# Kernel tuning notes

Measured on AMD Instinct MI355X. Metric: run time of the kernel, lower is better.

Reference implementation:

```python
import jax, jax.numpy as jnp
import numpy as np

B, S, D, H = 4, 2048, 1024, 16
HD = D // H


def setup_inputs() -> dict:
    key = jax.random.key(0)
    ks = jax.random.split(key, 12)
    inp = {
        "query": jax.random.normal(ks[0], (B, S, D), jnp.float32),
        "key": jax.random.normal(ks[1], (B, S, D), jnp.float32),
        "value": jax.random.normal(ks[2], (B, S, D), jnp.float32),
        "mask": jnp.tril(jnp.ones((S, S), jnp.int32)),  # causal mask
        "Wq": jax.random.normal(ks[3], (D, D), jnp.float32) / np.sqrt(D),
        "bq": jax.random.normal(ks[4], (D,), jnp.float32) * 0.02,
        "Wk": jax.random.normal(ks[5], (D, D), jnp.float32) / np.sqrt(D),
        "bk": jax.random.normal(ks[6], (D,), jnp.float32) * 0.02,
        "Wv": jax.random.normal(ks[7], (D, D), jnp.float32) / np.sqrt(D),
        "bv": jax.random.normal(ks[8], (D,), jnp.float32) * 0.02,
        "Wo": jax.random.normal(ks[9], (D, D), jnp.float32) / np.sqrt(D),
        "bo": jax.random.normal(ks[10], (D,), jnp.float32) * 0.02,
    }
    return inp


def reference(query, key, value, mask, Wq, bq, Wk, bk, Wv, bv, Wo, bo):
    # Linear projections (torch nn.Linear: y = x @ W.T + b)
    q = query @ Wq.T + bq
    k = key @ Wk.T + bk
    v = value @ Wv.T + bv
    # split heads: [B, S, D] -> [B, H, S, HD]
    q = q.reshape(B, S, H, HD).transpose(0, 2, 1, 3)
    k = k.reshape(B, S, H, HD).transpose(0, 2, 1, 3)
    v = v.reshape(B, S, H, HD).transpose(0, 2, 1, 3)
    # scaled dot-product attention with full [B,H,S,S] scores (faithful to source)
    scores = jnp.einsum("bhqd,bhkd->bhqk", q, k) / jnp.sqrt(jnp.float32(HD))
    scores = jnp.where(mask == 0, -jnp.inf, scores)
    attn = jax.nn.softmax(scores, axis=-1)
    out = jnp.einsum("bhqk,bhkd->bhqd", attn, v)
    # merge heads and output projection (dropout rate = 0.0 -> identity)
    out = out.transpose(0, 2, 1, 3).reshape(B, S, D)
    return out @ Wo.T + bo
```

## Files before the change

### kernel.cpp

```cpp
#include <hip/hip_runtime.h>

typedef __bf16 bf16x8 __attribute__((ext_vector_type(8)));
typedef __bf16 bf16x2 __attribute__((ext_vector_type(2)));
typedef float f32x4 __attribute__((ext_vector_type(4)));
typedef float f32x16 __attribute__((ext_vector_type(16)));
typedef unsigned short ushort;

__device__ __forceinline__ int4 cvt8(float4 a, float4 b) {
  bf16x8 v;
  v[0] = (__bf16)a.x; v[1] = (__bf16)a.y; v[2] = (__bf16)a.z; v[3] = (__bf16)a.w;
  v[4] = (__bf16)b.x; v[5] = (__bf16)b.y; v[6] = (__bf16)b.z; v[7] = (__bf16)b.w;
  return __builtin_bit_cast(int4, v);
}

__device__ __forceinline__ void gld16(const void* g, void* l) {
  __builtin_amdgcn_global_load_lds(
      (const __attribute__((address_space(1))) void*)g,
      (__attribute__((address_space(3))) void*)l, 16, 0, 0);
}

__device__ __forceinline__ unsigned pkbf(float a, float b) {
  bf16x2 v;
  v[0] = (__bf16)a;
  v[1] = (__bf16)b;
  return __builtin_bit_cast(unsigned, v);
}

#if __has_builtin(__builtin_amdgcn_permlane32_swap)
typedef unsigned u32x2 __attribute__((ext_vector_type(2)));
__device__ __forceinline__ void plswap(unsigned& a, unsigned& b, int hi) {
  (void)hi;
  u32x2 r = __builtin_amdgcn_permlane32_swap(a, b, false, false);
  a = r[0]; b = r[1];
}
#else
__device__ __forceinline__ void plswap(unsigned& a, unsigned& b, int hi) {
  const unsigned pa = (unsigned)__shfl_xor((int)a, 32);
  const unsigned pb = (unsigned)__shfl_xor((int)b, 32);
  const unsigned x = hi ? pb : a;
  const unsigned y = hi ? b : pa;
  a = x; b = y;
}
#endif

__device__ __forceinline__ f32x16 mfma32(bf16x8 a, bf16x8 b, f32x16 c) {
  return __builtin_amdgcn_mfma_f32_32x32x16_bf16(a, b, c, 0, 0, 0);
}

__global__ __launch_bounds__(256) void cvt4_k(const float* __restrict__ i0,
                                              const float* __restrict__ i1,
                                              const float* __restrict__ i2,
                                              const float* __restrict__ i3,
                                              ushort* __restrict__ o, int n8) {
  const int z = blockIdx.y;
  const float* in = (z == 0) ? i0 : (z == 1) ? i1 : (z == 2) ? i2 : i3;
  ushort* out = o + (size_t)z * 1024 * 1024;
  int i = blockIdx.x * 256 + threadIdx.x;
  if (i >= n8) return;
  const float4* p = (const float4*)in + (size_t)i * 2;
  *(int4*)(out + (size_t)i * 8) = cvt8(p[0], p[1]);
}

template <int AMODE, int WMODE, int OMODE>
__global__ __launch_bounds__(256) void gemm_k(const void* __restrict__ A,
                                              const void* __restrict__ W,
                                              const float* __restrict__ bias,
                                              void* __restrict__ Out,
                                              float oscale) {
  constexpr int K = 1024;
  __shared__ __align__(16) char lA[128 * 128];
  __shared__ __align__(16) char lB[128 * 128];
  const int t = threadIdx.x;
  const int l = t & 63;
  const int w = t >> 6;
  const int wr = w >> 1, wc = w & 1;
  const int m0 = blockIdx.x * 128;
  const int n0 = blockIdx.y * 128;
  const int srow = l >> 3;
  const int scol = ((l & 7) ^ srow) << 3;
  f32x4 acc[4][4];
#pragma unroll
  for (int i = 0; i < 4; ++i)
#pragma unroll
    for (int j = 0; j < 4; ++j) acc[i][j] = (f32x4){0.f, 0.f, 0.f, 0.f};

  for (int k0 = 0; k0 < K; k0 += 64) {
    if constexpr (AMODE == 1) {
#pragma unroll
      for (int i = 0; i < 4; ++i) {
        const int chunk = w * 4 + i;
        gld16((const ushort*)A + (size_t)(m0 + chunk * 8 + srow) * K + k0 + scol,
              lA + chunk * 1024);
      }
    } else {
#pragma unroll
      for (int qq = 0; qq < 4; ++qq) {
        const int L = t * 8 + qq * 2048;
        const int r = L >> 6, c = L & 63;
        const int dst = r * 128 + ((c * 2) ^ ((r & 7) << 4));
        const float* s0 = (const float*)A + (size_t)(m0 + r) * K + k0 + c;
        *(int4*)(lA + dst) = cvt8(*(const float4*)s0, *(const float4*)(s0 + 4));
      }
    }
    if constexpr (WMODE == 1) {
#pragma unroll
      for (int i = 0; i < 4; ++i) {
        const int chunk = w * 4 + i;
        gld16((const ushort*)W + (size_t)(n0 + chunk * 8 + srow) * K + k0 + scol,
              lB + chunk * 1024);
      }
    } else {
#pragma unroll
      for (int qq = 0; qq < 4; ++qq) {
        const int L = t * 8 + qq * 2048;
        const int r = L >> 6, c = L & 63;
        const int dst = r * 128 + ((c * 2) ^ ((r & 7) << 4));
        const float* s1 = (const float*)W + (size_t)(n0 + r) * K + k0 + c;
        *(int4*)(lB + dst) = cvt8(*(const float4*)s1, *(const float4*)(s1 + 4));
      }
    }
    __syncthreads();
#pragma unroll
    for (int ks = 0; ks < 2; ++ks) {
      const int kb = ks * 64 + ((l >> 4) << 4);
      bf16x8 af[4], bfv[4];
#pragma unroll
      for (int i = 0; i < 4; ++i) {
        const int row = wr * 64 + i * 16 + (l & 15);
        af[i] = *(const bf16x8*)(lA + row * 128 + (kb ^ ((row & 7) << 4)));
      }
#pragma unroll
      for (int j = 0; j < 4; ++j) {
        const int row = wc * 64 + j * 16 + (l & 15);
        bfv[j] = *(const bf16x8*)(lB + row * 128 + (kb ^ ((row & 7) << 4)));
      }
#pragma unroll
      for (int i = 0; i < 4; ++i)
#pragma unroll
        for (int j = 0; j < 4; ++j)
          acc[i][j] = __builtin_amdgcn_mfma_f32_16x16x32_bf16(af[i], bfv[j],
                                                              acc[i][j], 0, 0, 0);
    }
    __syncthreads();
  }
#pragma unroll
  for (int i = 0; i < 4; ++i)
#pragma unroll
    for (int j = 0; j < 4; ++j)
#pragma unroll
      for (int rg = 0; rg < 4; ++rg) {
        const int gm = m0 + wr * 64 + i * 16 + ((l >> 4) << 2) + rg;
        const int gn = n0 + wc * 64 + j * 16 + (l & 15);
        const float v = (acc[i][j][rg] + bias[gn]) * oscale;
        if constexpr (OMODE == 0) {
          const int b = gm >> 11, s = gm & 2047, h = gn >> 6, hd = gn & 63;
          ((ushort*)Out)[((((size_t)(b * 16 + h)) * 2048 + s) << 6) + hd] =
              __builtin_bit_cast(ushort, (__bf16)v);
        } else if constexpr (OMODE == 1) {
          const int b = gm >> 11, s = gm & 2047, h = gn >> 6, hd = gn & 63;
          ((ushort*)Out)[((((size_t)(b * 16 + h)) << 6) + hd) * 2048 + s] =
              __builtin_bit_cast(ushort, (__bf16)v);
        } else {
          ((float*)Out)[(size_t)gm * 1024 + gn] = v;
        }
      }
}

__global__ __launch_bounds__(256) void attn_k(const ushort* __restrict__ qh,
                                              const ushort* __restrict__ kh,
                                              const ushort* __restrict__ vth,
                                              ushort* __restrict__ out) {
  const int bh = blockIdx.x;
  const int qt = gridDim.y - 1 - blockIdx.y;
  const int q0 = qt * 128;
  const int t = threadIdx.x, l = t & 63, wv = t >> 6;
  const int lq = l & 31, hi = l >> 5;
  __shared__ __align__(16) char lk[2][64 * 128];
  __shared__ __align__(16) char lv[2][64 * 128];

  const int qrow = q0 + wv * 32 + lq;
  bf16x8 qf0, qf1, qf2, qf3;
  {
    const ushort* qp = qh + ((size_t)bh * 2048 + qrow) * 64 + hi * 8;
    qf0 = *(const bf16x8*)(qp);
    qf1 = *(const bf16x8*)(qp + 16);
    qf2 = *(const bf16x8*)(qp + 32);
    qf3 = *(const bf16x8*)(qp + 48);
  }
  bf16x8 ones8;
#pragma unroll
  for (int i = 0; i < 8; ++i) ones8[i] = (__bf16)1.0f;

  const int r0 = t >> 3;
  const int c0 = (t & 7) * 8;
  const ushort* kbase = kh + (size_t)bh * 2048 * 64 + (size_t)r0 * 64 + c0;
  const ushort* vbase = vth + (size_t)bh * 64 * 2048 + (size_t)r0 * 2048 + c0;
  const int dst0 = r0 * 128 + ((c0 * 2) ^ ((r0 & 7) << 4));

  int4 ka, kb2, va, vb2;
#define LOAD_TILE(kv0)                                            \
  do {                                                            \
    ka  = *(const int4*)(kbase + (size_t)(kv0) * 64);             \
    kb2 = *(const int4*)(kbase + (size_t)(kv0) * 64 + 32 * 64);   \
    va  = *(const int4*)(vbase + (kv0));                          \
    vb2 = *(const int4*)(vbase + (kv0) + 32 * 2048);              \
  } while (0)
#define WRITE_TILE(buf)                                           \
  do {                                                            \
    *(int4*)(lk[buf] + dst0) = ka;                                \
    *(int4*)(lk[buf] + dst0 + 32 * 128) = kb2;                    \
    *(int4*)(lv[buf] + dst0) = va;                                \
    *(int4*)(lv[buf] + dst0 + 32 * 128) = vb2;                    \
  } while (0)

  LOAD_TILE(0);
  WRITE_TILE(0);

  float m_r = -1e30f;
  f32x16 acco[2];
  f32x16 acc_l;
#pragma unroll
  for (int dt = 0; dt < 2; ++dt)
#pragma unroll
    for (int r = 0; r < 16; ++r) acco[dt][r] = 0.f;
#pragma unroll
  for (int r = 0; r < 16; ++r) acc_l[r] = 0.f;

  const int nt = 2 * qt + 2;
  int cur = 0;
#pragma unroll 1
  for (int ti = 0; ti < nt; ++ti) {
    __syncthreads();
    if (ti + 1 < nt) LOAD_TILE((ti + 1) << 6);

#pragma unroll
    for (int s = 0; s < 2; ++s) {
      const int kvs = (ti << 6) + s * 32;
      if (kvs > q0 + wv * 32 + 31) continue;

      f32x16 p;
#pragma unroll
      for (int r = 0; r < 16; ++r) p[r] = 0.f;
#pragma unroll
      for (int kd = 0; kd < 4; ++kd) {
        const int row = s * 32 + lq;
        const bf16x8 kf = *(const bf16x8*)(
            lk[cur] + row * 128 + ((kd * 32 + hi * 16) ^ ((row & 7) << 4)));
        const bf16x8 qf = (kd == 0) ? qf0 : (kd == 1) ? qf1 : (kd == 2) ? qf2 : qf3;
        p = mfma32(kf, qf, p);
      }
      if (kvs + 31 > q0 + wv * 32) {
#pragma unroll
        for (int r = 0; r < 16; ++r) {
          const int kv = kvs + (r & 3) + 8 * (r >> 2) + 4 * hi;
          if (kv > qrow) p[r] = -1e30f;
        }
      }
      const float a0 = fmaxf(fmaxf(p[0], p[1]), p[2]);
      const float a1 = fmaxf(fmaxf(p[3], p[4]), p[5]);
      const float a2 = fmaxf(fmaxf(p[6], p[7]), p[8]);
      const float a3 = fmaxf(fmaxf(p[9], p[10]), p[11]);
      const float a4 = fmaxf(fmaxf(p[12], p[13]), p[14]);
      const float b0 = fmaxf(fmaxf(a0, a1), a2);
      const float b1 = fmaxf(fmaxf(a3, a4), p[15]);
      float tm = fmaxf(b0, b1);
      tm = fmaxf(tm, __shfl_xor(tm, 32));
      if (!__all(tm <= m_r + 8.f)) {
        const float mn = fmaxf(m_r, tm);
        const float e = __builtin_amdgcn_exp2f(m_r - mn);
        m_r = mn;
#pragma unroll
        for (int dt = 0; dt < 2; ++dt)
#pragma unroll
          for (int r = 0; r < 16; ++r) acco[dt][r] *= e;
#pragma unroll
        for (int r = 0; r < 16; ++r) acc_l[r] *= e;
      }
#pragma unroll
      for (int r = 0; r < 16; ++r) p[r] = __builtin_amdgcn_exp2f(p[r] - m_r);
      unsigned W0a = pkbf(p[0], p[1]),   W0b = pkbf(p[2], p[3]);
      unsigned W1a = pkbf(p[4], p[5]),   W1b = pkbf(p[6], p[7]);
      unsigned W2a = pkbf(p[8], p[9]),   W2b = pkbf(p[10], p[11]);
      unsigned W3a = pkbf(p[12], p[13]), W3b = pkbf(p[14], p[15]);
#pragma unroll
      for (int ks = 0; ks < 2; ++ks) {
        unsigned a0u = ks ? W2a : W0a;
        unsigned a1u = ks ? W2b : W0b;
        unsigned b0u = ks ? W3a : W1a;
        unsigned b1u = ks ? W3b : W1b;
        plswap(a0u, b0u, hi);
        plswap(a1u, b1u, hi);
        const uint4 pw = {a0u, a1u, b0u, b1u};
        const bf16x8 pf = __builtin_bit_cast(bf16x8, pw);
        acc_l = mfma32(ones8, pf, acc_l);
#pragma unroll
        for (int dt = 0; dt < 2; ++dt) {
          const int row = dt * 32 + lq;
          const bf16x8 vf = *(const bf16x8*)(
              lv[cur] + row * 128 +
              ((s * 64 + ks * 32 + hi * 16) ^ ((row & 7) << 4)));
          acco[dt] = mfma32(vf, pf, acco[dt]);
        }
      }
    }
    if (ti + 1 < nt) WRITE_TILE(cur ^ 1);
    cur ^= 1;
  }
#undef LOAD_TILE
#undef WRITE_TILE
  const int b = bh >> 4, h = bh & 15;
  const float inv = __builtin_amdgcn_rcpf(acc_l[0]);
  ushort* orow = out + ((size_t)(b * 2048 + qrow)) * 1024 + h * 64;
#pragma unroll
  for (int dt = 0; dt < 2; ++dt)
#pragma unroll
    for (int g = 0; g < 4; ++g) {
      ushort4 st;
      st.x = __builtin_bit_cast(ushort, (__bf16)(acco[dt][4 * g + 0] * inv));
      st.y = __builtin_bit_cast(ushort, (__bf16)(acco[dt][4 * g + 1] * inv));
      st.z = __builtin_bit_cast(ushort, (__bf16)(acco[dt][4 * g + 2] * inv));
      st.w = __builtin_bit_cast(ushort, (__bf16)(acco[dt][4 * g + 3] * inv));
      *(ushort4*)(orow + dt * 32 + g * 8 + hi * 4) = st;
    }
}

extern "C" void kernel_launch(void* const* d_in, const int* in_sizes, int n_in,
                              void* d_out, int out_size, void* d_ws, size_t ws_size,
                              hipStream_t stream) {
  (void)in_sizes; (void)n_in; (void)out_size;
  const float* query = (const float*)d_in[0];
  const float* key = (const float*)d_in[1];
  const float* value = (const float*)d_in[2];
  const float* Wq = (const float*)d_in[4];
  const float* bq = (const float*)d_in[5];
  const float* Wk = (const float*)d_in[6];
  const float* bk = (const float*)d_in[7];
  const float* Wv = (const float*)d_in[8];
  const float* bv = (const float*)d_in[9];
  const float* Wo = (const float*)d_in[10];
  const float* bo = (const float*)d_in[11];

  char* ws = (char*)d_ws;
  const size_t SZA = (size_t)8192 * 1024 * 2;
  const size_t SZW = (size_t)1024 * 1024 * 2;
  ushort* qh = (ushort*)(ws + 0 * SZA);
  ushort* kh = (ushort*)(ws + 1 * SZA);
  ushort* vt = (ushort*)(ws + 2 * SZA);
  ushort* ao = (ushort*)(ws + 3 * SZA);
  dim3 bb(256), gg(64, 8), ga(64, 16);
  const float QS = 0.125f * 1.44269504088896f;

  if (ws_size >= 4 * SZA + 4 * SZW) {
    ushort* wq = (ushort*)(ws + 4 * SZA);
    ushort* wk = (ushort*)(ws + 4 * SZA + 1 * SZW);
    ushort* wv = (ushort*)(ws + 4 * SZA + 2 * SZW);
    ushort* wo = (ushort*)(ws + 4 * SZA + 3 * SZW);
    const int n8w = 1024 * 1024 / 8;
    hipLaunchKernelGGL(cvt4_k, dim3(n8w / 256, 4), bb, 0, stream, Wq, Wk, Wv, Wo, wq, n8w);
    hipLaunchKernelGGL((gemm_k<0, 1, 0>), gg, bb, 0, stream, (const void*)query, (const void*)wq, bq, (void*)qh, QS);
    hipLaunchKernelGGL((gemm_k<0, 1, 0>), gg, bb, 0, stream, (const void*)key, (const void*)wk, bk, (void*)kh, 1.0f);
    hipLaunchKernelGGL((gemm_k<0, 1, 1>), gg, bb, 0, stream, (const void*)value, (const void*)wv, bv, (void*)vt, 1.0f);
    hipLaunchKernelGGL(attn_k, ga, bb, 0, stream, qh, kh, vt, ao);
    hipLaunchKernelGGL((gemm_k<1, 1, 2>), gg, bb, 0, stream, (const void*)ao, (const void*)wo, bo, d_out, 1.0f);
  } else {
    hipLaunchKernelGGL((gemm_k<0, 0, 0>), gg, bb, 0, stream, (const void*)query, (const void*)Wq, bq, (void*)qh, QS);
    hipLaunchKernelGGL((gemm_k<0, 0, 0>), gg, bb, 0, stream, (const void*)key, (const void*)Wk, bk, (void*)kh, 1.0f);
    hipLaunchKernelGGL((gemm_k<0, 0, 1>), gg, bb, 0, stream, (const void*)value, (const void*)Wv, bv, (void*)vt, 1.0f);
    hipLaunchKernelGGL(attn_k, ga, bb, 0, stream, qh, kh, vt, ao);
    hipLaunchKernelGGL((gemm_k<1, 0, 2>), gg, bb, 0, stream, (const void*)ao, (const void*)Wo, bo, d_out, 1.0f);
  }
}
```

Baseline: 198.6 us.

## Merge QKV projections into one launch and rebalance causal attention blocks

The three input projections become a single launch with a z-dimension selecting Q/K/V, which cuts launch overhead and fills more of the GPU at once. Attention moves to 128-thread blocks with 64-row query tiles. Each block handles two tiles, one from the top and one from the bottom of the sequence, so causal work is balanced across blocks. The row-sum is now computed with shuffles and adds instead of an extra MFMA against a ones vector. The fallback path is restructured into a float-weight GEMM. Smaller attention blocks may lower per-block reuse of the K/V tiles held in LDS.

```diff
diff --git a/kernel.cpp b/kernel.cpp
--- a/kernel.cpp
+++ b/kernel.cpp
@@ -61,12 +61,305 @@
   *(int4*)(out + (size_t)i * 8) = cvt8(p[0], p[1]);
 }
 
-template <int AMODE, int WMODE, int OMODE>
-__global__ __launch_bounds__(256) void gemm_k(const void* __restrict__ A,
-                                              const void* __restrict__ W,
-                                              const float* __restrict__ bias,
-                                              void* __restrict__ Out,
-                                              float oscale) {
+template <int AMODE>
+__device__ __forceinline__ void gemm_body(const void* __restrict__ A,
+                                          const ushort* __restrict__ W,
+                                          const float* __restrict__ bias,
+                                          void* __restrict__ Out, float oscale,
+                                          int omode, char* lA, char* lB) {
+  constexpr int K = 1024;
+  const int t = threadIdx.x;
+  const int l = t & 63;
+  const int w = t >> 6;
+  const int wr = w >> 1, wc = w & 1;
+  const int m0 = blockIdx.x * 128;
+  const int n0 = blockIdx.y * 128;
+  const int srow = l >> 3;
+  const int scol = ((l & 7) ^ srow) << 3;
+  f32x4 acc[4][4];
+#pragma unroll
+  for (int i = 0; i < 4; ++i)
+#pragma unroll
+    for (int j = 0; j < 4; ++j) acc[i][j] = (f32x4){0.f, 0.f, 0.f, 0.f};
+
+  for (int k0 = 0; k0 < K; k0 += 64) {
+    if constexpr (AMODE == 1) {
+#pragma unroll
+      for (int i = 0; i < 4; ++i) {
+        const int chunk = w * 4 + i;
+        gld16((const ushort*)A + (size_t)(m0 + chunk * 8 + srow) * K + k0 + scol,
+              lA + chunk * 1024);
+      }
+    } else {
+#pragma unroll
+      for (int qq = 0; qq < 4; ++qq) {
+        const int L = t * 8 + qq * 2048;
+        const int r = L >> 6, c = L & 63;
+        const int dst = r * 128 + ((c * 2) ^ ((r & 7) << 4));
+        const float* s0 = (const float*)A + (size_t)(m0 + r) * K + k0 + c;
+        *(int4*)(lA + dst) = cvt8(*(const float4*)s0, *(const float4*)(s0 + 4));
+      }
+    }
+#pragma unroll
+    for (int i = 0; i < 4; ++i) {
+      const int chunk = w * 4 + i;
+      gld16(W + (size_t)(n0 + chunk * 8 + srow) * K + k0 + scol, lB + chunk * 1024);
+    }
+    __syncthreads();
+#pragma unroll
+    for (int ks = 0; ks < 2; ++ks) {
+      const int kb = ks * 64 + ((l >> 4) << 4);
+      bf16x8 af[4], bfv[4];
+#pragma unroll
+      for (int i = 0; i < 4; ++i) {
+        const int row = wr * 64 + i * 16 + (l & 15);
+        af[i] = *(const bf16x8*)(lA + row * 128 + (kb ^ ((row & 7) << 4)));
+      }
+#pragma unroll
+      for (int j = 0; j < 4; ++j) {
+        const int row = wc * 64 + j * 16 + (l & 15);
+        bfv[j] = *(const bf16x8*)(lB + row * 128 + (kb ^ ((row & 7) << 4)));
+      }
+#pragma unroll
+      for (int i = 0; i < 4; ++i)
+#pragma unroll
+        for (int j = 0; j < 4; ++j)
+          acc[i][j] = __builtin_amdgcn_mfma_f32_16x16x32_bf16(af[i], bfv[j],
+                                                              acc[i][j], 0, 0, 0);
+    }
+    __syncthreads();
+  }
+#pragma unroll
+  for (int i = 0; i < 4; ++i)
+#pragma unroll
+    for (int j = 0; j < 4; ++j)
+#pragma unroll
+      for (int rg = 0; rg < 4; ++rg) {
+        const int gm = m0 + wr * 64 + i * 16 + ((l >> 4) << 2) + rg;
+        const int gn = n0 + wc * 64 + j * 16 + (l & 15);
+        const float v = (acc[i][j][rg] + bias[gn]) * oscale;
+        if (omode == 0) {
+          const int b = gm >> 11, s = gm & 2047, h = gn >> 6, hd = gn & 63;
+          ((ushort*)Out)[((((size_t)(b * 16 + h)) * 2048 + s) << 6) + hd] =
+              __builtin_bit_cast(ushort, (__bf16)v);
+        } else if (omode == 1) {
+          const int b = gm >> 11, s = gm & 2047, h = gn >> 6, hd = gn & 63;
+          ((ushort*)Out)[((((size_t)(b * 16 + h)) << 6) + hd) * 2048 + s] =
+              __builtin_bit_cast(ushort, (__bf16)v);
+        } else {
+          ((float*)Out)[(size_t)gm * 1024 + gn] = v;
+        }
+      }
+}
+
+__global__ __launch_bounds__(256) void gemmQKV_k(
+    const float* __restrict__ Aq, const float* __restrict__ Ak,
+    const float* __restrict__ Av, const ushort* __restrict__ Wb,
+    const float* __restrict__ bq, const float* __restrict__ bk,
+    const float* __restrict__ bv, ushort* __restrict__ qh,
+    ushort* __restrict__ kh, ushort* __restrict__ vt, float qs) {
+  __shared__ __align__(16) char lA[128 * 128];
+  __shared__ __align__(16) char lB[128 * 128];
+  const int z = blockIdx.z;
+  const float* A = (z == 0) ? Aq : (z == 1) ? Ak : Av;
+  const float* bias = (z == 0) ? bq : (z == 1) ? bk : bv;
+  void* Out = (z == 0) ? (void*)qh : (z == 1) ? (void*)kh : (void*)vt;
+  gemm_body<0>(A, Wb + (size_t)z * 1024 * 1024, bias, Out,
+               (z == 0) ? qs : 1.0f, (z == 2) ? 1 : 0, lA, lB);
+}
+
+__global__ __launch_bounds__(256) void gemmO_k(const ushort* __restrict__ A,
+                                               const ushort* __restrict__ W,
+                                               const float* __restrict__ bias,
+                                               float* __restrict__ Out) {
+  __shared__ __align__(16) char lA[128 * 128];
+  __shared__ __align__(16) char lB[128 * 128];
+  gemm_body<1>(A, W, bias, Out, 1.0f, 2, lA, lB);
+}
+
+__global__ __launch_bounds__(128) void attn_k(const ushort* __restrict__ qh,
+                                              const ushort* __restrict__ kh,
+                                              const ushort* __restrict__ vth,
+                                              ushort* __restrict__ out) {
+  const int bh = blockIdx.x;
+  const int t = threadIdx.x, l = t & 63, wv = t >> 6;
+  const int lq = l & 31, hi = l >> 5;
+  __shared__ __align__(16) char lk[2][64 * 128];
+  __shared__ __align__(16) char lv[2][64 * 128];
+
+  const int r0 = t >> 1;
+  const int cq = (t & 1) * 32;
+  const ushort* kbase = kh + (size_t)bh * 2048 * 64 + (size_t)r0 * 64 + cq;
+  const ushort* vbase = vth + (size_t)bh * 64 * 2048 + (size_t)r0 * 2048 + cq;
+  const int swz = (r0 & 7) << 4;
+  const int d0 = r0 * 128 + ((cq * 2 + 0) ^ swz);
+  const int d1 = r0 * 128 + ((cq * 2 + 16) ^ swz);
+  const int d2 = r0 * 128 + ((cq * 2 + 32) ^ swz);
+  const int d3 = r0 * 128 + ((cq * 2 + 48) ^ swz);
+  const int b = bh >> 4, h = bh & 15;
+
+  int4 ka0, ka1, ka2, ka3, va0, va1, va2, va3;
+#define LOAD_TILE(kv0)                                      \
+  do {                                                      \
+    const ushort* kp = kbase + (size_t)(kv0) * 64;          \
+    const ushort* vp = vbase + (kv0);                       \
+    ka0 = *(const int4*)(kp);                               \
+    ka1 = *(const int4*)(kp + 8);                           \
+    ka2 = *(const int4*)(kp + 16);                          \
+    ka3 = *(const int4*)(kp + 24);                          \
+    va0 = *(const int4*)(vp);                               \
+    va1 = *(const int4*)(vp + 8);                           \
+    va2 = *(const int4*)(vp + 16);                          \
+    va3 = *(const int4*)(vp + 24);                          \
+  } while (0)
+#define WRITE_TILE(buf)                                     \
+  do {                                                      \
+    *(int4*)(lk[buf] + d0) = ka0;                           \
+    *(int4*)(lk[buf] + d1) = ka1;                           \
+    *(int4*)(lk[buf] + d2) = ka2;                           \
+    *(int4*)(lk[buf] + d3) = ka3;                           \
+    *(int4*)(lv[buf] + d0) = va0;                           \
+    *(int4*)(lv[buf] + d1) = va1;                           \
+    *(int4*)(lv[buf] + d2) = va2;                           \
+    *(int4*)(lv[buf] + d3) = va3;                           \
+  } while (0)
+
+#pragma unroll 1
+  for (int pass = 0; pass < 2; ++pass) {
+    const int qt = pass ? blockIdx.y : (31 - blockIdx.y);
+    const int q0 = qt * 64;
+    const int qwave = q0 + wv * 32;
+    const int qrow = qwave + lq;
+
+    bf16x8 qf0, qf1, qf2, qf3;
+    {
+      const ushort* qp = qh + ((size_t)bh * 2048 + qrow) * 64 + hi * 8;
+      qf0 = *(const bf16x8*)(qp);
+      qf1 = *(const bf16x8*)(qp + 16);
+      qf2 = *(const bf16x8*)(qp + 32);
+      qf3 = *(const bf16x8*)(qp + 48);
+    }
+    LOAD_TILE(0);
+    __syncthreads();
+    WRITE_TILE(0);
+
+    float m_r = -1e30f, l_r = 0.f;
+    f32x16 acco[2];
+#pragma unroll
+    for (int dt = 0; dt < 2; ++dt)
+#pragma unroll
+      for (int r = 0; r < 16; ++r) acco[dt][r] = 0.f;
+
+    const int nt = qt + 1;
+    int cur = 0;
+#pragma unroll 1
+    for (int ti = 0; ti < nt; ++ti) {
+      __syncthreads();
+      if (ti + 1 < nt) LOAD_TILE((ti + 1) << 6);
+
+#pragma unroll
+      for (int s = 0; s < 2; ++s) {
+        const int kvs = (ti << 6) + s * 32;
+        if (kvs > qwave + 31) continue;
+
+        f32x16 p;
+#pragma unroll
+        for (int r = 0; r < 16; ++r) p[r] = 0.f;
+#pragma unroll
+        for (int kd = 0; kd < 4; ++kd) {
+          const int row = s * 32 + lq;
+          const bf16x8 kf = *(const bf16x8*)(
+              lk[cur] + row * 128 + ((kd * 32 + hi * 16) ^ ((row & 7) << 4)));
+          const bf16x8 qf = (kd == 0) ? qf0 : (kd == 1) ? qf1 : (kd == 2) ? qf2 : qf3;
+          p = mfma32(kf, qf, p);
+        }
+        if (kvs + 31 > qwave) {
+#pragma unroll
+          for (int r = 0; r < 16; ++r) {
+            const int kv = kvs + (r & 3) + 8 * (r >> 2) + 4 * hi;
+            if (kv > qrow) p[r] = -1e30f;
+          }
+        }
+        const float a0 = fmaxf(fmaxf(p[0], p[1]), p[2]);
+        const float a1 = fmaxf(fmaxf(p[3], p[4]), p[5]);
+        const float a2 = fmaxf(fmaxf(p[6], p[7]), p[8]);
+        const float a3 = fmaxf(fmaxf(p[9], p[10]), p[11]);
+        const float a4 = fmaxf(fmaxf(p[12], p[13]), p[14]);
+        const float b0 = fmaxf(fmaxf(a0, a1), a2);
+        const float b1 = fmaxf(fmaxf(a3, a4), p[15]);
+        float tm = fmaxf(b0, b1);
+        tm = fmaxf(tm, __shfl_xor(tm, 32));
+        if (!__all(tm <= m_r + 8.f)) {
+          const float mn = fmaxf(m_r, tm);
+          const float e = __builtin_amdgcn_exp2f(m_r - mn);
+          m_r = mn;
+          l_r *= e;
+#pragma unroll
+          for (int dt = 0; dt < 2; ++dt)
+#pragma unroll
+            for (int r = 0; r < 16; ++r) acco[dt][r] *= e;
+        }
+#pragma unroll
+        for (int r = 0; r < 16; ++r) p[r] = __builtin_amdgcn_exp2f(p[r] - m_r);
+        float sr[8];
+#pragma unroll
+        for (int r = 0; r < 8; ++r) sr[r] = p[r] + p[r + 8];
+#pragma unroll
+        for (int r = 0; r < 4; ++r) sr[r] = sr[r] + sr[r + 4];
+        float rs = (sr[0] + sr[1]) + (sr[2] + sr[3]);
+        rs += __shfl_xor(rs, 32);
+        l_r += rs;
+        unsigned W0a = pkbf(p[0], p[1]),   W0b = pkbf(p[2], p[3]);
+        unsigned W1a = pkbf(p[4], p[5]),   W1b = pkbf(p[6], p[7]);
+        unsigned W2a = pkbf(p[8], p[9]),   W2b = pkbf(p[10], p[11]);
+        unsigned W3a = pkbf(p[12], p[13]), W3b = pkbf(p[14], p[15]);
+#pragma unroll
+        for (int ks = 0; ks < 2; ++ks) {
+          unsigned a0u = ks ? W2a : W0a;
+          unsigned a1u = ks ? W2b : W0b;
+          unsigned b0u = ks ? W3a : W1a;
+          unsigned b1u = ks ? W3b : W1b;
+          plswap(a0u, b0u, hi);
+          plswap(a1u, b1u, hi);
+          const uint4 pw = {a0u, a1u, b0u, b1u};
+          const bf16x8 pf = __builtin_bit_cast(bf16x8, pw);
+#pragma unroll
+          for (int dt = 0; dt < 2; ++dt) {
+            const int row = dt * 32 + lq;
+            const bf16x8 vf = *(const bf16x8*)(
+                lv[cur] + row * 128 +
+                ((s * 64 + ks * 32 + hi * 16) ^ ((row & 7) << 4)));
+            acco[dt] = mfma32(vf, pf, acco[dt]);
+          }
+        }
+      }
+      if (ti + 1 < nt) WRITE_TILE(cur ^ 1);
+      cur ^= 1;
+    }
+    const float inv = __builtin_amdgcn_rcpf(l_r);
+    ushort* orow = out + ((size_t)(b * 2048 + qrow)) * 1024 + h * 64;
+#pragma unroll
+    for (int dt = 0; dt < 2; ++dt)
+#pragma unroll
+      for (int g = 0; g < 4; ++g) {
+        ushort4 st;
+        st.x = __builtin_bit_cast(ushort, (__bf16)(acco[dt][4 * g + 0] * inv));
+        st.y = __builtin_bit_cast(ushort, (__bf16)(acco[dt][4 * g + 1] * inv));
+        st.z = __builtin_bit_cast(ushort, (__bf16)(acco[dt][4 * g + 2] * inv));
+        st.w = __builtin_bit_cast(ushort, (__bf16)(acco[dt][4 * g + 3] * inv));
+        *(ushort4*)(orow + dt * 32 + g * 8 + hi * 4) = st;
+      }
+  }
+#undef LOAD_TILE
+#undef WRITE_TILE
+}
+
+template <int OMODE>
+__global__ __launch_bounds__(256) void gemmF_k(const void* __restrict__ A,
+                                               const float* __restrict__ W,
+                                               const float* __restrict__ bias,
+                                               void* __restrict__ Out,
+                                               float oscale, int amode) {
   constexpr int K = 1024;
   __shared__ __align__(16) char lA[128 * 128];
   __shared__ __align__(16) char lB[128 * 128];
@@ -76,48 +369,26 @@
   const int wr = w >> 1, wc = w & 1;
   const int m0 = blockIdx.x * 128;
   const int n0 = blockIdx.y * 128;
-  const int srow = l >> 3;
-  const int scol = ((l & 7) ^ srow) << 3;
   f32x4 acc[4][4];
 #pragma unroll
   for (int i = 0; i < 4; ++i)
 #pragma unroll
     for (int j = 0; j < 4; ++j) acc[i][j] = (f32x4){0.f, 0.f, 0.f, 0.f};
-
   for (int k0 = 0; k0 < K; k0 += 64) {
-    if constexpr (AMODE == 1) {
-#pragma unroll
-      for (int i = 0; i < 4; ++i) {
-        const int chunk = w * 4 + i;
-        gld16((const ushort*)A + (size_t)(m0 + chunk * 8 + srow) * K + k0 + scol,
-              lA + chunk * 1024);
-      }
-    } else {
-#pragma unroll
-      for (int qq = 0; qq < 4; ++qq) {
-        const int L = t * 8 + qq * 2048;
-        const int r = L >> 6, c = L & 63;
-        const int dst = r * 128 + ((c * 2) ^ ((r & 7) << 4));
+#pragma unroll
+    for (int qq = 0; qq < 4; ++qq) {
+      const int L = t * 8 + qq * 2048;
+      const int r = L >> 6, c = L & 63;
+      const int dst = r * 128 + ((c * 2) ^ ((r & 7) << 4));
+      if (amode == 0) {
         const float* s0 = (const float*)A + (size_t)(m0 + r) * K + k0 + c;
         *(int4*)(lA + dst) = cvt8(*(const float4*)s0, *(const float4*)(s0 + 4));
-      }
-    }
-    if constexpr (WMODE == 1) {
-#pragma unroll
-      for (int i = 0; i < 4; ++i) {
-        const int chunk = w * 4 + i;
-        gld16((const ushort*)W + (size_t)(n0 + chunk * 8 + srow) * K + k0 + scol,
-              lB + chunk * 1024);
-      }
-    } else {
-#pragma unroll
-      for (int qq = 0; qq < 4; ++qq) {
-        const int L = t * 8 + qq * 2048;
-        const int r = L >> 6, c = L & 63;
-        const int dst = r * 128 + ((c * 2) ^ ((r & 7) << 4));
-        const float* s1 = (const float*)W + (size_t)(n0 + r) * K + k0 + c;
-        *(int4*)(lB + dst) = cvt8(*(const float4*)s1, *(const float4*)(s1 + 4));
-      }
+      } else {
+        *(int4*)(lA + dst) =
+            *(const int4*)((const ushort*)A + (size_t)(m0 + r) * K + k0 + c);
+      }
+      const float* s1 = W + (size_t)(n0 + r) * K + k0 + c;
+      *(int4*)(lB + dst) = cvt8(*(const float4*)s1, *(const float4*)(s1 + 4));
     }
     __syncthreads();
 #pragma unroll
@@ -164,164 +435,6 @@
           ((float*)Out)[(size_t)gm * 1024 + gn] = v;
         }
       }
-}
-
-__global__ __launch_bounds__(256) void attn_k(const ushort* __restrict__ qh,
-                                              const ushort* __restrict__ kh,
-                                              const ushort* __restrict__ vth,
-                                              ushort* __restrict__ out) {
-  const int bh = blockIdx.x;
-  const int qt = gridDim.y - 1 - blockIdx.y;
-  const int q0 = qt * 128;
-  const int t = threadIdx.x, l = t & 63, wv = t >> 6;
-  const int lq = l & 31, hi = l >> 5;
-  __shared__ __align__(16) char lk[2][64 * 128];
-  __shared__ __align__(16) char lv[2][64 * 128];
-
-  const int qrow = q0 + wv * 32 + lq;
-  bf16x8 qf0, qf1, qf2, qf3;
-  {
-    const ushort* qp = qh + ((size_t)bh * 2048 + qrow) * 64 + hi * 8;
-    qf0 = *(const bf16x8*)(qp);
-    qf1 = *(const bf16x8*)(qp + 16);
-    qf2 = *(const bf16x8*)(qp + 32);
-    qf3 = *(const bf16x8*)(qp + 48);
-  }
-  bf16x8 ones8;
-#pragma unroll
-  for (int i = 0; i < 8; ++i) ones8[i] = (__bf16)1.0f;
-
-  const int r0 = t >> 3;
-  const int c0 = (t & 7) * 8;
-  const ushort* kbase = kh + (size_t)bh * 2048 * 64 + (size_t)r0 * 64 + c0;
-  const ushort* vbase = vth + (size_t)bh * 64 * 2048 + (size_t)r0 * 2048 + c0;
-  const int dst0 = r0 * 128 + ((c0 * 2) ^ ((r0 & 7) << 4));
-
-  int4 ka, kb2, va, vb2;
-#define LOAD_TILE(kv0)                                            \
-  do {                                                            \
-    ka  = *(const int4*)(kbase + (size_t)(kv0) * 64);             \
-    kb2 = *(const int4*)(kbase + (size_t)(kv0) * 64 + 32 * 64);   \
-    va  = *(const int4*)(vbase + (kv0));                          \
-    vb2 = *(const int4*)(vbase + (kv0) + 32 * 2048);              \
-  } while (0)
-#define WRITE_TILE(buf)                                           \
-  do {                                                            \
-    *(int4*)(lk[buf] + dst0) = ka;                                \
-    *(int4*)(lk[buf] + dst0 + 32 * 128) = kb2;                    \
-    *(int4*)(lv[buf] + dst0) = va;                                \
-    *(int4*)(lv[buf] + dst0 + 32 * 128) = vb2;                    \
-  } while (0)
-
-  LOAD_TILE(0);
-  WRITE_TILE(0);
-
-  float m_r = -1e30f;
-  f32x16 acco[2];
-  f32x16 acc_l;
-#pragma unroll
-  for (int dt = 0; dt < 2; ++dt)
-#pragma unroll
-    for (int r = 0; r < 16; ++r) acco[dt][r] = 0.f;
-#pragma unroll
-  for (int r = 0; r < 16; ++r) acc_l[r] = 0.f;
-
-  const int nt = 2 * qt + 2;
-  int cur = 0;
-#pragma unroll 1
-  for (int ti = 0; ti < nt; ++ti) {
-    __syncthreads();
-    if (ti + 1 < nt) LOAD_TILE((ti + 1) << 6);
-
-#pragma unroll
-    for (int s = 0; s < 2; ++s) {
-      const int kvs = (ti << 6) + s * 32;
-      if (kvs > q0 + wv * 32 + 31) continue;
-
-      f32x16 p;
-#pragma unroll
-      for (int r = 0; r < 16; ++r) p[r] = 0.f;
-#pragma unroll
-      for (int kd = 0; kd < 4; ++kd) {
-        const int row = s * 32 + lq;
-        const bf16x8 kf = *(const bf16x8*)(
-            lk[cur] + row * 128 + ((kd * 32 + hi * 16) ^ ((row & 7) << 4)));
-        const bf16x8 qf = (kd == 0) ? qf0 : (kd == 1) ? qf1 : (kd == 2) ? qf2 : qf3;
-        p = mfma32(kf, qf, p);
-      }
-      if (kvs + 31 > q0 + wv * 32) {
-#pragma unroll
-        for (int r = 0; r < 16; ++r) {
-          const int kv = kvs + (r & 3) + 8 * (r >> 2) + 4 * hi;
-          if (kv > qrow) p[r] = -1e30f;
-        }
-      }
-      const float a0 = fmaxf(fmaxf(p[0], p[1]), p[2]);
-      const float a1 = fmaxf(fmaxf(p[3], p[4]), p[5]);
-      const float a2 = fmaxf(fmaxf(p[6], p[7]), p[8]);
-      const float a3 = fmaxf(fmaxf(p[9], p[10]), p[11]);
-      const float a4 = fmaxf(fmaxf(p[12], p[13]), p[14]);
-      const float b0 = fmaxf(fmaxf(a0, a1), a2);
-      const float b1 = fmaxf(fmaxf(a3, a4), p[15]);
-      float tm = fmaxf(b0, b1);
-      tm = fmaxf(tm, __shfl_xor(tm, 32));
-      if (!__all(tm <= m_r + 8.f)) {
-        const float mn = fmaxf(m_r, tm);
-        const float e = __builtin_amdgcn_exp2f(m_r - mn);
-        m_r = mn;
-#pragma unroll
-        for (int dt = 0; dt < 2; ++dt)
-#pragma unroll
-          for (int r = 0; r < 16; ++r) acco[dt][r] *= e;
-#pragma unroll
-        for (int r = 0; r < 16; ++r) acc_l[r] *= e;
-      }
-#pragma unroll
-      for (int r = 0; r < 16; ++r) p[r] = __builtin_amdgcn_exp2f(p[r] - m_r);
-      unsigned W0a = pkbf(p[0], p[1]),   W0b = pkbf(p[2], p[3]);
-      unsigned W1a = pkbf(p[4], p[5]),   W1b = pkbf(p[6], p[7]);
-      unsigned W2a = pkbf(p[8], p[9]),   W2b = pkbf(p[10], p[11]);
-      unsigned W3a = pkbf(p[12], p[13]), W3b = pkbf(p[14], p[15]);
-#pragma unroll
-      for (int ks = 0; ks < 2; ++ks) {
-        unsigned a0u = ks ? W2a : W0a;
-        unsigned a1u = ks ? W2b : W0b;
-        unsigned b0u = ks ? W3a : W1a;
-        unsigned b1u = ks ? W3b : W1b;
-        plswap(a0u, b0u, hi);
-        plswap(a1u, b1u, hi);
-        const uint4 pw = {a0u, a1u, b0u, b1u};
-        const bf16x8 pf = __builtin_bit_cast(bf16x8, pw);
-        acc_l = mfma32(ones8, pf, acc_l);
-#pragma unroll
-        for (int dt = 0; dt < 2; ++dt) {
-          const int row = dt * 32 + lq;
-          const bf16x8 vf = *(const bf16x8*)(
-              lv[cur] + row * 128 +
-              ((s * 64 + ks * 32 + hi * 16) ^ ((row & 7) << 4)));
-          acco[dt] = mfma32(vf, pf, acco[dt]);
-        }
-      }
-    }
-    if (ti + 1 < nt) WRITE_TILE(cur ^ 1);
-    cur ^= 1;
-  }
-#undef LOAD_TILE
-#undef WRITE_TILE
-  const int b = bh >> 4, h = bh & 15;
-  const float inv = __builtin_amdgcn_rcpf(acc_l[0]);
-  ushort* orow = out + ((size_t)(b * 2048 + qrow)) * 1024 + h * 64;
-#pragma unroll
-  for (int dt = 0; dt < 2; ++dt)
-#pragma unroll
-    for (int g = 0; g < 4; ++g) {
-      ushort4 st;
-      st.x = __builtin_bit_cast(ushort, (__bf16)(acco[dt][4 * g + 0] * inv));
-      st.y = __builtin_bit_cast(ushort, (__bf16)(acco[dt][4 * g + 1] * inv));
-      st.z = __builtin_bit_cast(ushort, (__bf16)(acco[dt][4 * g + 2] * inv));
-      st.w = __builtin_bit_cast(ushort, (__bf16)(acco[dt][4 * g + 3] * inv));
-      *(ushort4*)(orow + dt * 32 + g * 8 + hi * 4) = st;
-    }
 }
 
 extern "C" void kernel_launch(void* const* d_in, const int* in_sizes, int n_in,
@@ -347,26 +460,24 @@
   ushort* kh = (ushort*)(ws + 1 * SZA);
   ushort* vt = (ushort*)(ws + 2 * SZA);
   ushort* ao = (ushort*)(ws + 3 * SZA);
-  dim3 bb(256), gg(64, 8), ga(64, 16);
+  dim3 gg(64, 8);
   const float QS = 0.125f * 1.44269504088896f;
 
   if (ws_size >= 4 * SZA + 4 * SZW) {
     ushort* wq = (ushort*)(ws + 4 * SZA);
-    ushort* wk = (ushort*)(ws + 4 * SZA + 1 * SZW);
-    ushort* wv = (ushort*)(ws + 4 * SZA + 2 * SZW);
     ushort* wo = (ushort*)(ws + 4 * SZA + 3 * SZW);
     const int n8w = 1024 * 1024 / 8;
-    hipLaunchKernelGGL(cvt4_k, dim3(n8w / 256, 4), bb, 0, stream, Wq, Wk, Wv, Wo, wq, n8w);
-    hipLaunchKernelGGL((gemm_k<0, 1, 0>), gg, bb, 0, stream, (const void*)query, (const void*)wq, bq, (void*)qh, QS);
-    hipLaunchKernelGGL((gemm_k<0, 1, 0>), gg, bb, 0, stream, (const void*)key, (const void*)wk, bk, (void*)kh, 1.0f);
-    hipLaunchKernelGGL((gemm_k<0, 1, 1>), gg, bb, 0, stream, (const void*)value, (const void*)wv, bv, (void*)vt, 1.0f);
-    hipLaunchKernelGGL(attn_k, ga, bb, 0, stream, qh, kh, vt, ao);
-    hipLaunchKernelGGL((gemm_k<1, 1, 2>), gg, bb, 0, stream, (const void*)ao, (const void*)wo, bo, d_out, 1.0f);
+    hipLaunchKernelGGL(cvt4_k, dim3(n8w / 256, 4), dim3(256), 0, stream,
+                       Wq, Wk, Wv, Wo, wq, n8w);
+    hipLaunchKernelGGL(gemmQKV_k, dim3(64, 8, 3), dim3(256), 0, stream,
+                       query, key, value, wq, bq, bk, bv, qh, kh, vt, QS);
+    hipLaunchKernelGGL(attn_k, dim3(64, 16), dim3(128), 0, stream, qh, kh, vt, ao);
+    hipLaunchKernelGGL(gemmO_k, gg, dim3(256), 0, stream, ao, wo, bo, (float*)d_out);
   } else {
-    hipLaunchKernelGGL((gemm_k<0, 0, 0>), gg, bb, 0, stream, (const void*)query, (const void*)Wq, bq, (void*)qh, QS);
-    hipLaunchKernelGGL((gemm_k<0, 0, 0>), gg, bb, 0, stream, (const void*)key, (const void*)Wk, bk, (void*)kh, 1.0f);
-    hipLaunchKernelGGL((gemm_k<0, 0, 1>), gg, bb, 0, stream, (const void*)value, (const void*)Wv, bv, (void*)vt, 1.0f);
-    hipLaunchKernelGGL(attn_k, ga, bb, 0, stream, qh, kh, vt, ao);
-    hipLaunchKernelGGL((gemm_k<1, 0, 2>), gg, bb, 0, stream, (const void*)ao, (const void*)Wo, bo, d_out, 1.0f);
+    hipLaunchKernelGGL((gemmF_k<0>), gg, dim3(256), 0, stream, (const void*)query, Wq, bq, (void*)qh, QS, 0);
+    hipLaunchKernelGGL((gemmF_k<0>), gg, dim3(256), 0, stream, (const void*)key, Wk, bk, (void*)kh, 1.0f, 0);
+    hipLaunchKernelGGL((gemmF_k<1>), gg, dim3(256), 0, stream, (const void*)value, Wv, bv, (void*)vt, 1.0f, 0);
+    hipLaunchKernelGGL(attn_k, dim3(64, 16), dim3(128), 0, stream, qh, kh, vt, ao);
+    hipLaunchKernelGGL((gemmF_k<2>), gg, dim3(256), 0, stream, (const void*)ao, Wo, bo, d_out, 1.0f, 1);
   }
 }
```

New measurement: 205.8 us. 1.04x slower.
